# Kernel tuning notes

Measured on AMD Instinct MI355X. Metric: run time of the kernel, lower is better.

Reference implementation:

```python
import jax, jax.numpy as jnp
import numpy as np


def _up2(x):
    return jnp.repeat(jnp.repeat(x, 2, axis=2), 2, axis=3)


def setup_inputs() -> dict:
    key = jax.random.key(0)
    ks = jax.random.split(key, 6)
    Vps, C, H, W = 32, 128, 64, 64
    return {
        "x1": jax.random.normal(ks[0], (Vps, C, H, W), dtype=jnp.float32),
        "x2": jax.random.normal(ks[1], (Vps, C, H // 2, W // 2), dtype=jnp.float32),
        "x3": jax.random.normal(ks[2], (Vps, C, H // 4, W // 4), dtype=jnp.float32),
        "x4": jax.random.normal(ks[3], (Vps, C, H // 4, W // 4), dtype=jnp.float32),
        "conv_w": jax.random.normal(ks[4], (128, 512), dtype=jnp.float32) * 0.02,
        "conv_b": jnp.zeros((128,), dtype=jnp.float32),
        "gamma": jnp.zeros((1,), dtype=jnp.float32),
        "weight": jnp.ones((128,), dtype=jnp.float32),
        "lin_w": jax.random.normal(ks[5], (1, 128), dtype=jnp.float32) * 0.1,
    }


def reference(x1, x2, x3, x4, conv_w, conv_b, gamma, weight, lin_w):
    # upsample lower pyramid levels to x1 resolution and concat on channels
    x_sm = jnp.concatenate([x1, _up2(x2), _up2(_up2(x3)), _up2(_up2(x4))], axis=1)
    # 1x1 conv: [Vps,512,H,W] x [128,512] -> [Vps,128,H,W]
    x_sm = jnp.einsum('vchw,oc->vohw', x_sm, conv_w) + conv_b[None, :, None, None]
    Vps, C, H, W = x_sm.shape

    # --- batch (viewport) attention ---
    gap = jnp.mean(x_sm, axis=(2, 3))                     # [Vps, C]
    v_q = gap @ lin_w.T                                    # [Vps, 1]
    att = v_q @ v_q.T                                      # [Vps, Vps]
    att_new = jnp.broadcast_to(jnp.max(att, axis=-1, keepdims=True), att.shape)
    vps_mat = jax.nn.softmax(att_new, axis=-1)             # rows constant -> uniform
    v_v = x_sm.reshape(Vps, C * H * W)
    vps_att = (vps_mat @ v_v).reshape(Vps, C, H, W)
    x_sm = vps_att * gamma + x_sm

    # --- channel attention ---
    c_q = jnp.mean(x_sm, axis=(2, 3))                      # [Vps, C]
    att_C = c_q.T @ c_q                                    # [C, C]
    C_mat = jax.nn.softmax(att_C, axis=-1) * weight        # broadcast over last dim
    c_v = x_sm.reshape(C, Vps * H * W)                     # faithful raw reshape as in torch
    C_att = (C_mat @ c_v).reshape(Vps, C, H, W)
    out = C_att + x_sm
    return out.reshape(Vps, C, H * W)
```

## Files before the change

kernel.cpp:

```cpp
#include <hip/hip_runtime.h>

#define V 32
#define CH 128
#define SP 4096

typedef __attribute__((ext_vector_type(8))) short bf16x8;
typedef __attribute__((ext_vector_type(4))) float f32x4;

__device__ __forceinline__ unsigned short bf16rne(float x) {
    union { float f; unsigned u; } v; v.f = x;
    unsigned r = v.u + 0x7fff + ((v.u >> 16) & 1);
    return (unsigned short)(r >> 16);
}

__device__ __forceinline__ int xswz(int s) { return (s & 7) ^ ((s >> 2) & 7); }

__device__ __forceinline__ const float* xsm_row(const float* xsm, int j, int r) {
    return xsm + ((size_t)((j >> 2) * CH + (j & 3) * 32 + r)) * SP;
}

__global__ __launch_bounds__(256) void prep_w(const float* __restrict__ W,
                                              unsigned short* __restrict__ Wpad)
{
    int row = blockIdx.x;
    int j = threadIdx.x;
    if (j < 136) {
        int sigma = row >> 7, o = row & 127;
        float v = (j < 128) ? W[o * 512 + sigma * 128 + j] : 0.f;
        Wpad[row * 136 + j] = bf16rne(v);
    }
}

__global__ __launch_bounds__(256) void conv_lo(
    const float* __restrict__ xa, const float* __restrict__ xb,
    const unsigned short* __restrict__ WA, const unsigned short* __restrict__ WB,
    int spatial, int nph, float* __restrict__ outbuf)
{
    __shared__ __align__(16) unsigned short Wl[128 * 136];
    __shared__ __align__(16) unsigned short Xl[64 * 128];
    const int v = blockIdx.y, sc = blockIdx.x, tid = threadIdx.x;
    const int lane = tid & 63, w = tid >> 6;
    const int l15 = lane & 15, quad = lane >> 4;
    const int o0 = (w >> 1) * 64, s0 = (w & 1) * 32;
    const int sq = tid & 15, cp0 = tid >> 4;

    f32x4 acc[4][2];
#pragma unroll
    for (int it = 0; it < 4; ++it)
#pragma unroll
        for (int st = 0; st < 2; ++st) acc[it][st] = (f32x4){0.f, 0.f, 0.f, 0.f};

#pragma unroll 1
    for (int ph = 0; ph < nph; ++ph) {
        if (ph) __syncthreads();
        const float* xp = ph ? xb : xa;
        const unsigned short* wp = ph ? WB : WA;
        {
            const float4* wsrc = (const float4*)wp;
            float4* wdst = (float4*)Wl;
            for (int idx = tid; idx < 2176; idx += 256) wdst[idx] = wsrc[idx];
        }
        const float* xbase = xp + (size_t)v * CH * spatial + sc * 64;
#pragma unroll
        for (int rep = 0; rep < 4; ++rep) {
            int c = (cp0 + rep * 16) * 2;
            const float* r0 = xbase + (size_t)c * spatial + sq * 4;
            float4 va = *(const float4*)r0;
            float4 vb = *(const float4*)(r0 + spatial);
            float a4[4] = {va.x, va.y, va.z, va.w};
            float b4[4] = {vb.x, vb.y, vb.z, vb.w};
#pragma unroll
            for (int i = 0; i < 4; ++i) {
                int s = sq * 4 + i;
                ushort2 pk; pk.x = bf16rne(a4[i]); pk.y = bf16rne(b4[i]);
                *(ushort2*)&Xl[s * 128 + (((c >> 3) ^ xswz(s)) * 8) + (c & 7)] = pk;
            }
        }
        __syncthreads();
#pragma unroll
        for (int ks = 0; ks < 4; ++ks) {
            int kb = ks * 4 + quad;
            bf16x8 af[4], bfr[2];
#pragma unroll
            for (int it = 0; it < 4; ++it)
                af[it] = *(const bf16x8*)&Wl[(o0 + it * 16 + l15) * 136 + ks * 32 + quad * 8];
#pragma unroll
            for (int st = 0; st < 2; ++st) {
                int s = s0 + st * 16 + l15;
                bfr[st] = *(const bf16x8*)&Xl[s * 128 + ((kb ^ xswz(s)) * 8)];
            }
#pragma unroll
            for (int it = 0; it < 4; ++it)
#pragma unroll
                for (int st = 0; st < 2; ++st)
                    acc[it][st] = __builtin_amdgcn_mfma_f32_16x16x32_bf16(
                        af[it], bfr[st], acc[it][st], 0, 0, 0);
        }
    }
#pragma unroll
    for (int it = 0; it < 4; ++it)
#pragma unroll
        for (int reg = 0; reg < 4; ++reg) {
            int o = o0 + it * 16 + quad * 4 + reg;
            float* orow = outbuf + ((size_t)(v * CH + o)) * spatial + sc * 64;
#pragma unroll
            for (int st = 0; st < 2; ++st) {
                int s_l = s0 + st * 16 + l15;
                orow[s_l] = acc[it][st][reg];
            }
        }
}

__global__ __launch_bounds__(256) void conv_full(
    const float* __restrict__ x1, const unsigned short* __restrict__ W0,
    const float* __restrict__ bias, const float* __restrict__ conv2,
    const float* __restrict__ conv34, float* __restrict__ xsm,
    float* __restrict__ gap)
{
    __shared__ __align__(16) unsigned short Wl[128 * 136];
    __shared__ __align__(16) unsigned short Xl[64 * 128];
    __shared__ float gscr[4][64];
    const int v = blockIdx.y, sc = blockIdx.x, tid = threadIdx.x;
    const int lane = tid & 63, w = tid >> 6;
    const int l15 = lane & 15, quad = lane >> 4;
    const int o0 = (w >> 1) * 64, s0 = (w & 1) * 32;
    const int sq = tid & 15, cp0 = tid >> 4;

    f32x4 acc[4][2];
#pragma unroll
    for (int it = 0; it < 4; ++it)
#pragma unroll
        for (int st = 0; st < 2; ++st) acc[it][st] = (f32x4){0.f, 0.f, 0.f, 0.f};

    {
        const float4* wsrc = (const float4*)W0;
        float4* wdst = (float4*)Wl;
        for (int idx = tid; idx < 2176; idx += 256) wdst[idx] = wsrc[idx];
    }
    const float* xbase = x1 + (size_t)v * CH * SP + sc * 64;
#pragma unroll
    for (int rep = 0; rep < 4; ++rep) {
        int c = (cp0 + rep * 16) * 2;
        const float* r0 = xbase + (size_t)c * SP + sq * 4;
        float4 va = *(const float4*)r0;
        float4 vb = *(const float4*)(r0 + SP);
        float a4[4] = {va.x, va.y, va.z, va.w};
        float b4[4] = {vb.x, vb.y, vb.z, vb.w};
#pragma unroll
        for (int i = 0; i < 4; ++i) {
            int s = sq * 4 + i;
            ushort2 pk; pk.x = bf16rne(a4[i]); pk.y = bf16rne(b4[i]);
            *(ushort2*)&Xl[s * 128 + (((c >> 3) ^ xswz(s)) * 8) + (c & 7)] = pk;
        }
    }
    __syncthreads();
#pragma unroll
    for (int ks = 0; ks < 4; ++ks) {
        int kb = ks * 4 + quad;
        bf16x8 af[4], bfr[2];
#pragma unroll
        for (int it = 0; it < 4; ++it)
            af[it] = *(const bf16x8*)&Wl[(o0 + it * 16 + l15) * 136 + ks * 32 + quad * 8];
#pragma unroll
        for (int st = 0; st < 2; ++st) {
            int s = s0 + st * 16 + l15;
            bfr[st] = *(const bf16x8*)&Xl[s * 128 + ((kb ^ xswz(s)) * 8)];
        }
#pragma unroll
        for (int it = 0; it < 4; ++it)
#pragma unroll
            for (int st = 0; st < 2; ++st)
                acc[it][st] = __builtin_amdgcn_mfma_f32_16x16x32_bf16(
                    af[it], bfr[st], acc[it][st], 0, 0, 0);
    }

    const float* c2row = conv2 + (size_t)v * CH * 1024 + (sc >> 1) * 32;
    const float* c34row = conv34 + (size_t)v * CH * 256 + (sc >> 2) * 16;
    float gs[16];
#pragma unroll
    for (int it = 0; it < 4; ++it)
#pragma unroll
        for (int reg = 0; reg < 4; ++reg) {
            int o = o0 + it * 16 + quad * 4 + reg;
            float b = bias[o];
            float* orow = xsm + ((size_t)(v * CH + o)) * SP + sc * 64;
            const float* c2p = c2row + (size_t)o * 1024;
            const float* c34p = c34row + (size_t)o * 256;
            float lsum = 0.f;
#pragma unroll
            for (int st = 0; st < 2; ++st) {
                int s_l = s0 + st * 16 + l15;
                float val = acc[it][st][reg] + b + c2p[s_l >> 1] + c34p[s_l >> 2];
                orow[s_l] = val;
                lsum += val;
            }
            gs[it * 4 + reg] = lsum;
        }
#pragma unroll
    for (int m = 1; m < 16; m <<= 1)
#pragma unroll
        for (int k = 0; k < 16; ++k) gs[k] += __shfl_xor(gs[k], m, 64);
    if (l15 == 0) {
#pragma unroll
        for (int it = 0; it < 4; ++it)
#pragma unroll
            for (int reg = 0; reg < 4; ++reg)
                gscr[w][it * 16 + quad * 4 + reg] = gs[it * 4 + reg];
    }
    __syncthreads();
    if (tid < 128) {
        int o = tid, b2 = (o >> 6) * 2;
        atomicAdd(&gap[v * CH + o], gscr[b2][o & 63] + gscr[b2 + 1][o & 63]);
    }
}

__global__ __launch_bounds__(128) void build_G(
    const float* __restrict__ gap, const float* __restrict__ gammap,
    const float* __restrict__ weight, unsigned short* __restrict__ GsPad)
{
    __shared__ float cq[32][128];
    __shared__ float red[128];
    const int i = blockIdx.x, j = threadIdx.x;
    const float g = gammap[0];

    float gb = 0.f;
    for (int v = 0; v < 32; ++v) gb += gap[v * CH + j];
    gb = gb * (1.f / 32.f) * (1.f / 4096.f) * g;
    for (int v = 0; v < 32; ++v) cq[v][j] = gap[v * CH + j] * (1.f / 4096.f) + gb;
    __syncthreads();

    float a = 0.f;
    for (int v = 0; v < 32; ++v) a += cq[v][i] * cq[v][j];

    red[j] = a; __syncthreads();
    float m = -1e30f;
    for (int t = 0; t < 128; ++t) m = fmaxf(m, red[t]);
    __syncthreads();
    float e = __expf(a - m);
    red[j] = e; __syncthreads();
    float ssum = 0.f;
    for (int t = 0; t < 128; ++t) ssum += red[t];
    float cm = e / ssum * weight[j] + ((i == j) ? 1.f : 0.f);
    __syncthreads();
    red[j] = cm; __syncthreads();
    float rs = 0.f;
    for (int t = (j & 3); t < 128; t += 4) rs += red[t];
    float gfull = cm + g * (1.f / 32.f) * rs;
    GsPad[i * 136 + j] = bf16rne(gfull - ((i == j) ? 1.f : 0.f));
}

__global__ __launch_bounds__(256) void apply_G(
    float* __restrict__ xsm, const unsigned short* __restrict__ GsPad)
{
    __shared__ __align__(16) unsigned short Gl[128 * 136];
    __shared__ __align__(16) unsigned short Xl[64 * 128];
    const int r = blockIdx.y, sc = blockIdx.x, tid = threadIdx.x;
    const int lane = tid & 63, w = tid >> 6;
    const int l15 = lane & 15, quad = lane >> 4;
    const int i0 = (w >> 1) * 64, s0 = (w & 1) * 32;
    const int sq = tid & 15, cp0 = tid >> 4;

    f32x4 acc[4][2];
#pragma unroll
    for (int it = 0; it < 4; ++it)
#pragma unroll
        for (int st = 0; st < 2; ++st) acc[it][st] = (f32x4){0.f, 0.f, 0.f, 0.f};

    {
        const float4* gsrc = (const float4*)GsPad;
        float4* gdst = (float4*)Gl;
        for (int idx = tid; idx < 2176; idx += 256) gdst[idx] = gsrc[idx];
    }
#pragma unroll
    for (int rep = 0; rep < 4; ++rep) {
        int c = (cp0 + rep * 16) * 2;
        const float* r0 = xsm_row(xsm, c, r) + sc * 64 + sq * 4;
        const float* r1 = xsm_row(xsm, c + 1, r) + sc * 64 + sq * 4;
        float4 va = *(const float4*)r0;
        float4 vb = *(const float4*)r1;
        float a4[4] = {va.x, va.y, va.z, va.w};
        float b4[4] = {vb.x, vb.y, vb.z, vb.w};
#pragma unroll
        for (int i = 0; i < 4; ++i) {
            int s = sq * 4 + i;
            ushort2 pk; pk.x = bf16rne(a4[i]); pk.y = bf16rne(b4[i]);
            *(ushort2*)&Xl[s * 128 + (((c >> 3) ^ xswz(s)) * 8) + (c & 7)] = pk;
        }
    }
    __syncthreads();
#pragma unroll
    for (int ks = 0; ks < 4; ++ks) {
        int kb = ks * 4 + quad;
        bf16x8 af[4], bfr[2];
#pragma unroll
        for (int it = 0; it < 4; ++it)
            af[it] = *(const bf16x8*)&Gl[(i0 + it * 16 + l15) * 136 + ks * 32 + quad * 8];
#pragma unroll
        for (int st = 0; st < 2; ++st) {
            int s = s0 + st * 16 + l15;
            bfr[st] = *(const bf16x8*)&Xl[s * 128 + ((kb ^ xswz(s)) * 8)];
        }
#pragma unroll
        for (int it = 0; it < 4; ++it)
#pragma unroll
            for (int st = 0; st < 2; ++st)
                acc[it][st] = __builtin_amdgcn_mfma_f32_16x16x32_bf16(
                    af[it], bfr[st], acc[it][st], 0, 0, 0);
    }
#pragma unroll
    for (int it = 0; it < 4; ++it)
#pragma unroll
        for (int reg = 0; reg < 4; ++reg) {
            int i = i0 + it * 16 + quad * 4 + reg;
            float* rowp = (float*)xsm_row(xsm, i, r) + sc * 64;
#pragma unroll
            for (int st = 0; st < 2; ++st) {
                int s_l = s0 + st * 16 + l15;
                rowp[s_l] = rowp[s_l] + acc[it][st][reg];
            }
        }
}

extern "C" void kernel_launch(void* const* d_in, const int* in_sizes, int n_in,
                              void* d_out, int out_size, void* d_ws, size_t ws_size,
                              hipStream_t stream)
{
    const float* x1     = (const float*)d_in[0];
    const float* x2     = (const float*)d_in[1];
    const float* x3     = (const float*)d_in[2];
    const float* x4     = (const float*)d_in[3];
    const float* conv_w = (const float*)d_in[4];
    const float* conv_b = (const float*)d_in[5];
    const float* gamma  = (const float*)d_in[6];
    const float* weight = (const float*)d_in[7];

    float* out = (float*)d_out;
    float* ws  = (float*)d_ws;

    float* conv2  = ws;
    float* conv34 = ws + (size_t)4194304;
    float* gap    = ws + (size_t)5242880;
    unsigned short* Wpad  = (unsigned short*)(ws + (size_t)5246976);
    unsigned short* GsPad = (unsigned short*)(ws + (size_t)5281792);

    hipMemsetAsync(gap, 0, 4096 * sizeof(float), stream);

    prep_w<<<512, 256, 0, stream>>>(conv_w, Wpad);
    conv_lo<<<dim3(16, 32), 256, 0, stream>>>(x2, x2, Wpad + 1 * 128 * 136,
                                              Wpad + 1 * 128 * 136, 1024, 1, conv2);
    conv_lo<<<dim3(4, 32), 256, 0, stream>>>(x3, x4, Wpad + 2 * 128 * 136,
                                             Wpad + 3 * 128 * 136, 256, 2, conv34);
    conv_full<<<dim3(64, 32), 256, 0, stream>>>(x1, Wpad, conv_b, conv2, conv34, out, gap);
    build_G<<<128, 128, 0, stream>>>(gap, gamma, weight, GsPad);
    apply_G<<<dim3(64, 32), 256, 0, stream>>>(out, GsPad);
}
```

Measured before the change: 215.3 us.

## Read weights from global instead of LDS and swap MFMA operands for vector stores

Drops the shared-memory staging of the 128x136 bf16 weight/G matrices in the three GEMM kernels and loads MFMA A fragments straight from global (cached) memory. LDS use falls to the X tile only, and the launch bounds now request 4 blocks per CU to raise occupancy. MFMA operands are swapped so each lane holds 4 consecutive spatial outputs, which allows float4 stores and read-modify-writes and changes the gap reduction shuffle pattern. The cost is repeated global/L2 weight fetches per wave in place of LDS reads.

```diff
diff --git a/kernel.cpp b/kernel.cpp
--- a/kernel.cpp
+++ b/kernel.cpp
@@ -31,12 +31,11 @@
     }
 }
 
-__global__ __launch_bounds__(256) void conv_lo(
+__global__ __launch_bounds__(256, 4) void conv_lo(
     const float* __restrict__ xa, const float* __restrict__ xb,
     const unsigned short* __restrict__ WA, const unsigned short* __restrict__ WB,
     int spatial, int nph, float* __restrict__ outbuf)
 {
-    __shared__ __align__(16) unsigned short Wl[128 * 136];
     __shared__ __align__(16) unsigned short Xl[64 * 128];
     const int v = blockIdx.y, sc = blockIdx.x, tid = threadIdx.x;
     const int lane = tid & 63, w = tid >> 6;
@@ -55,11 +54,6 @@
         if (ph) __syncthreads();
         const float* xp = ph ? xb : xa;
         const unsigned short* wp = ph ? WB : WA;
-        {
-            const float4* wsrc = (const float4*)wp;
-            float4* wdst = (float4*)Wl;
-            for (int idx = tid; idx < 2176; idx += 256) wdst[idx] = wsrc[idx];
-        }
         const float* xbase = xp + (size_t)v * CH * spatial + sc * 64;
 #pragma unroll
         for (int rep = 0; rep < 4; ++rep) {
@@ -83,7 +77,7 @@
             bf16x8 af[4], bfr[2];
 #pragma unroll
             for (int it = 0; it < 4; ++it)
-                af[it] = *(const bf16x8*)&Wl[(o0 + it * 16 + l15) * 136 + ks * 32 + quad * 8];
+                af[it] = *(const bf16x8*)&wp[(o0 + it * 16 + l15) * 136 + ks * 32 + quad * 8];
 #pragma unroll
             for (int st = 0; st < 2; ++st) {
                 int s = s0 + st * 16 + l15;
@@ -94,30 +88,27 @@
 #pragma unroll
                 for (int st = 0; st < 2; ++st)
                     acc[it][st] = __builtin_amdgcn_mfma_f32_16x16x32_bf16(
-                        af[it], bfr[st], acc[it][st], 0, 0, 0);
-        }
-    }
-#pragma unroll
-    for (int it = 0; it < 4; ++it)
-#pragma unroll
-        for (int reg = 0; reg < 4; ++reg) {
-            int o = o0 + it * 16 + quad * 4 + reg;
-            float* orow = outbuf + ((size_t)(v * CH + o)) * spatial + sc * 64;
-#pragma unroll
-            for (int st = 0; st < 2; ++st) {
-                int s_l = s0 + st * 16 + l15;
-                orow[s_l] = acc[it][st][reg];
-            }
-        }
-}
-
-__global__ __launch_bounds__(256) void conv_full(
+                        bfr[st], af[it], acc[it][st], 0, 0, 0);
+        }
+    }
+#pragma unroll
+    for (int it = 0; it < 4; ++it) {
+        int o = o0 + it * 16 + l15;
+        float* orow = outbuf + ((size_t)(v * CH + o)) * spatial + sc * 64;
+#pragma unroll
+        for (int st = 0; st < 2; ++st) {
+            int sb = s0 + st * 16 + quad * 4;
+            *(f32x4*)(orow + sb) = acc[it][st];
+        }
+    }
+}
+
+__global__ __launch_bounds__(256, 4) void conv_full(
     const float* __restrict__ x1, const unsigned short* __restrict__ W0,
     const float* __restrict__ bias, const float* __restrict__ conv2,
     const float* __restrict__ conv34, float* __restrict__ xsm,
     float* __restrict__ gap)
 {
-    __shared__ __align__(16) unsigned short Wl[128 * 136];
     __shared__ __align__(16) unsigned short Xl[64 * 128];
     __shared__ float gscr[4][64];
     const int v = blockIdx.y, sc = blockIdx.x, tid = threadIdx.x;
@@ -132,11 +123,6 @@
 #pragma unroll
         for (int st = 0; st < 2; ++st) acc[it][st] = (f32x4){0.f, 0.f, 0.f, 0.f};
 
-    {
-        const float4* wsrc = (const float4*)W0;
-        float4* wdst = (float4*)Wl;
-        for (int idx = tid; idx < 2176; idx += 256) wdst[idx] = wsrc[idx];
-    }
     const float* xbase = x1 + (size_t)v * CH * SP + sc * 64;
 #pragma unroll
     for (int rep = 0; rep < 4; ++rep) {
@@ -160,7 +146,7 @@
         bf16x8 af[4], bfr[2];
 #pragma unroll
         for (int it = 0; it < 4; ++it)
-            af[it] = *(const bf16x8*)&Wl[(o0 + it * 16 + l15) * 136 + ks * 32 + quad * 8];
+            af[it] = *(const bf16x8*)&W0[(o0 + it * 16 + l15) * 136 + ks * 32 + quad * 8];
 #pragma unroll
         for (int st = 0; st < 2; ++st) {
             int s = s0 + st * 16 + l15;
@@ -171,41 +157,44 @@
 #pragma unroll
             for (int st = 0; st < 2; ++st)
                 acc[it][st] = __builtin_amdgcn_mfma_f32_16x16x32_bf16(
-                    af[it], bfr[st], acc[it][st], 0, 0, 0);
+                    bfr[st], af[it], acc[it][st], 0, 0, 0);
     }
 
     const float* c2row = conv2 + (size_t)v * CH * 1024 + (sc >> 1) * 32;
     const float* c34row = conv34 + (size_t)v * CH * 256 + (sc >> 2) * 16;
-    float gs[16];
-#pragma unroll
-    for (int it = 0; it < 4; ++it)
-#pragma unroll
-        for (int reg = 0; reg < 4; ++reg) {
-            int o = o0 + it * 16 + quad * 4 + reg;
-            float b = bias[o];
-            float* orow = xsm + ((size_t)(v * CH + o)) * SP + sc * 64;
-            const float* c2p = c2row + (size_t)o * 1024;
-            const float* c34p = c34row + (size_t)o * 256;
-            float lsum = 0.f;
-#pragma unroll
-            for (int st = 0; st < 2; ++st) {
-                int s_l = s0 + st * 16 + l15;
-                float val = acc[it][st][reg] + b + c2p[s_l >> 1] + c34p[s_l >> 2];
-                orow[s_l] = val;
-                lsum += val;
-            }
-            gs[it * 4 + reg] = lsum;
-        }
-#pragma unroll
-    for (int m = 1; m < 16; m <<= 1)
-#pragma unroll
-        for (int k = 0; k < 16; ++k) gs[k] += __shfl_xor(gs[k], m, 64);
-    if (l15 == 0) {
-#pragma unroll
-        for (int it = 0; it < 4; ++it)
-#pragma unroll
-            for (int reg = 0; reg < 4; ++reg)
-                gscr[w][it * 16 + quad * 4 + reg] = gs[it * 4 + reg];
+    float gs[4];
+#pragma unroll
+    for (int it = 0; it < 4; ++it) {
+        int o = o0 + it * 16 + l15;
+        float b = bias[o];
+        float* orow = xsm + ((size_t)(v * CH + o)) * SP + sc * 64;
+        const float* c2p = c2row + (size_t)o * 1024;
+        const float* c34p = c34row + (size_t)o * 256;
+        float lsum = 0.f;
+#pragma unroll
+        for (int st = 0; st < 2; ++st) {
+            int sb = s0 + st * 16 + quad * 4;
+            float2 c2v = *(const float2*)(c2p + (sb >> 1));
+            float c34v = c34p[sb >> 2];
+            f32x4 a = acc[it][st];
+            f32x4 ov;
+            ov[0] = a[0] + b + c2v.x + c34v;
+            ov[1] = a[1] + b + c2v.x + c34v;
+            ov[2] = a[2] + b + c2v.y + c34v;
+            ov[3] = a[3] + b + c2v.y + c34v;
+            *(f32x4*)(orow + sb) = ov;
+            lsum += ov[0] + ov[1] + ov[2] + ov[3];
+        }
+        gs[it] = lsum;
+    }
+#pragma unroll
+    for (int m = 16; m < 64; m <<= 1)
+#pragma unroll
+        for (int k = 0; k < 4; ++k) gs[k] += __shfl_xor(gs[k], m, 64);
+    if (quad == 0) {
+#pragma unroll
+        for (int it = 0; it < 4; ++it)
+            gscr[w][it * 16 + l15] = gs[it];
     }
     __syncthreads();
     if (tid < 128) {
@@ -249,10 +238,9 @@
     GsPad[i * 136 + j] = bf16rne(gfull - ((i == j) ? 1.f : 0.f));
 }
 
-__global__ __launch_bounds__(256) void apply_G(
+__global__ __launch_bounds__(256, 4) void apply_G(
     float* __restrict__ xsm, const unsigned short* __restrict__ GsPad)
 {
-    __shared__ __align__(16) unsigned short Gl[128 * 136];
     __shared__ __align__(16) unsigned short Xl[64 * 128];
     const int r = blockIdx.y, sc = blockIdx.x, tid = threadIdx.x;
     const int lane = tid & 63, w = tid >> 6;
@@ -266,11 +254,6 @@
 #pragma unroll
         for (int st = 0; st < 2; ++st) acc[it][st] = (f32x4){0.f, 0.f, 0.f, 0.f};
 
-    {
-        const float4* gsrc = (const float4*)GsPad;
-        float4* gdst = (float4*)Gl;
-        for (int idx = tid; idx < 2176; idx += 256) gdst[idx] = gsrc[idx];
-    }
 #pragma unroll
     for (int rep = 0; rep < 4; ++rep) {
         int c = (cp0 + rep * 16) * 2;
@@ -294,7 +277,7 @@
         bf16x8 af[4], bfr[2];
 #pragma unroll
         for (int it = 0; it < 4; ++it)
-            af[it] = *(const bf16x8*)&Gl[(i0 + it * 16 + l15) * 136 + ks * 32 + quad * 8];
+            af[it] = *(const bf16x8*)&GsPad[(i0 + it * 16 + l15) * 136 + ks * 32 + quad * 8];
 #pragma unroll
         for (int st = 0; st < 2; ++st) {
             int s = s0 + st * 16 + l15;
@@ -305,20 +288,20 @@
 #pragma unroll
             for (int st = 0; st < 2; ++st)
                 acc[it][st] = __builtin_amdgcn_mfma_f32_16x16x32_bf16(
-                    af[it], bfr[st], acc[it][st], 0, 0, 0);
-    }
-#pragma unroll
-    for (int it = 0; it < 4; ++it)
-#pragma unroll
-        for (int reg = 0; reg < 4; ++reg) {
-            int i = i0 + it * 16 + quad * 4 + reg;
-            float* rowp = (float*)xsm_row(xsm, i, r) + sc * 64;
-#pragma unroll
-            for (int st = 0; st < 2; ++st) {
-                int s_l = s0 + st * 16 + l15;
-                rowp[s_l] = rowp[s_l] + acc[it][st][reg];
-            }
-        }
+                    bfr[st], af[it], acc[it][st], 0, 0, 0);
+    }
+#pragma unroll
+    for (int it = 0; it < 4; ++it) {
+        int i = i0 + it * 16 + l15;
+        float* rowp = (float*)xsm_row(xsm, i, r) + sc * 64;
+#pragma unroll
+        for (int st = 0; st < 2; ++st) {
+            int sb = s0 + st * 16 + quad * 4;
+            f32x4 res = *(const f32x4*)(rowp + sb);
+            res += acc[it][st];
+            *(f32x4*)(rowp + sb) = res;
+        }
+    }
 }
 
 extern "C" void kernel_launch(void* const* d_in, const int* in_sizes, int n_in,
```

Result: slower. 230.7 us (+7.1%).
